# Performance work log

Measured on AMD Instinct MI355X. Metric: run time of the kernel, lower is better.

Reference implementation:

```python
import jax, jax.numpy as jnp
import numpy as np

N, D, C, G, NNZ = 256, 1024, 50000, 4, 300000
EPS = 1e-5


def setup_inputs() -> dict:
    key = jax.random.key(0)
    ks = jax.random.split(key, 5)
    return {
        "output": jax.random.normal(ks[0], (N, D), jnp.float32),
        "wt2_w": jax.random.normal(ks[1], (C, D), jnp.float32) * 0.02,
        "wt2_b": jnp.zeros((C,), jnp.float32),
        "A_vals": jax.random.uniform(ks[2], (G, NNZ), dtype=jnp.float32),
        "vec": jnp.ones((G,), jnp.float32),
        "A_rows": jax.random.randint(ks[3], (G, NNZ), 0, C, jnp.int32),
        "A_cols": jax.random.randint(ks[4], (G, NNZ), 0, C, jnp.int32),
    }


def reference(output, wt2_w, wt2_b, A_vals, vec, A_rows, A_cols):
    # BatchNorm1d(embed_dim, affine=False), training-mode batch stats (biased var)
    mean = jnp.mean(output, axis=0)
    var = jnp.var(output, axis=0)
    h0 = (output - mean) * jax.lax.rsqrt(var + EPS)
    # wt2 linear + swish -> Z [N, C]
    h1 = h0 @ wt2_w.T + wt2_b
    Z = h1 * jax.nn.sigmoid(h1)
    # multi-graph sparse propagation: neighbors += spmm(A_i * vec[i], Z^T)^T
    # spmm out[b, r] = sum_{e: rows[e]==r} vals[e] * Z[b, cols[e]]
    Zt = Z.T  # [C, N]
    neighbors = jnp.zeros_like(Z)
    n_graphs = A_vals.shape[0]
    for i in range(n_graphs):  # small fixed number of relation graphs
        vals = A_vals[i] * vec[i]               # learnable per-graph weight
        msgs = Zt[A_cols[i]] * vals[:, None]    # [nnz, N] gathered messages
        agg = jax.ops.segment_sum(msgs, A_rows[i], num_segments=Zt.shape[0])  # [C, N]
        neighbors = neighbors + agg.T
    # residual combine
    return neighbors + Z
```

## Files before the change

### kernel.cpp

```cpp
#include <hip/hip_runtime.h>

typedef __attribute__((ext_vector_type(8))) short short8;
typedef __attribute__((ext_vector_type(4))) float floatx4;

#define C_DIM 50000
#define D_DIM 1024
#define N_DIM 256
#define G_NUM 4
#define NNZ_G 300000
#define E_TOT (G_NUM * NNZ_G)

#define O_SB   0u
#define O_H0   8192u
#define O_ZT   532480u
#define O_CNT  26132480u
#define O_OFF  26332544u
#define O_CUR  26532608u
#define O_BS   26732672u
#define O_EDG  26733696u

static __device__ __forceinline__ unsigned short f2bf(float f) {
    union { float f; unsigned u; } v; v.f = f;
    unsigned r = v.u + 0x7fffu + ((v.u >> 16) & 1u);
    return (unsigned short)(r >> 16);
}
static __device__ __forceinline__ float bf2f(unsigned short u) {
    union { unsigned u; float f; } v; v.u = ((unsigned)u) << 16;
    return v.f;
}

__global__ __launch_bounds__(256) void k_bnstats(const float* __restrict__ x,
                                                 float* __restrict__ scale,
                                                 float* __restrict__ bias) {
    int d = blockIdx.x * 256 + threadIdx.x;
    float s = 0.f, ss = 0.f;
    for (int n = 0; n < N_DIM; ++n) {
        float v = x[n * D_DIM + d];
        s += v; ss += v * v;
    }
    float mean = s * (1.f / N_DIM);
    float var  = ss * (1.f / N_DIM) - mean * mean;
    float sc = rsqrtf(var + 1e-5f);
    scale[d] = sc;
    bias[d] = -mean * sc;
}

__global__ __launch_bounds__(256) void k_h0(const float* __restrict__ x,
                                            const float* __restrict__ scale,
                                            const float* __restrict__ bias,
                                            unsigned short* __restrict__ h0) {
    int id = blockIdx.x * 256 + threadIdx.x;
    int d = id & (D_DIM - 1);
    h0[id] = f2bf(x[id] * scale[d] + bias[d]);
}

__global__ __launch_bounds__(256) void k_gemm(const float* __restrict__ W,
                                              const float* __restrict__ wb,
                                              const unsigned short* __restrict__ h0,
                                              unsigned short* __restrict__ Zt) {
    __shared__ unsigned short As[64 * 40];
    __shared__ unsigned short Bs[256 * 40];
    const int t = threadIdx.x;
    const int c0 = blockIdx.x * 64;
    const int w = t >> 6, lane = t & 63;
    const int m = lane & 15, g = lane >> 4;
    const int arow = t >> 2, aseg = t & 3;

    floatx4 acc[4][4];
#pragma unroll
    for (int i = 0; i < 4; ++i)
#pragma unroll
        for (int j = 0; j < 4; ++j) acc[i][j] = (floatx4)0.f;

    for (int kk = 0; kk < D_DIM; kk += 32) {
        {
            int c = c0 + arow;
            float4 f0, f1;
            if (c < C_DIM) {
                const float4* src = (const float4*)&W[(size_t)c * D_DIM + kk + aseg * 8];
                f0 = src[0]; f1 = src[1];
            } else {
                f0 = f1 = make_float4(0.f, 0.f, 0.f, 0.f);
            }
            unsigned p0 = (unsigned)f2bf(f0.x) | ((unsigned)f2bf(f0.y) << 16);
            unsigned p1 = (unsigned)f2bf(f0.z) | ((unsigned)f2bf(f0.w) << 16);
            unsigned p2 = (unsigned)f2bf(f1.x) | ((unsigned)f2bf(f1.y) << 16);
            unsigned p3 = (unsigned)f2bf(f1.z) | ((unsigned)f2bf(f1.w) << 16);
            *(uint4*)&As[arow * 40 + aseg * 8] = make_uint4(p0, p1, p2, p3);
        }
        {
            const uint4* src = (const uint4*)&h0[(size_t)t * D_DIM + kk];
            uint4* dst = (uint4*)&Bs[t * 40];
            dst[0] = src[0]; dst[1] = src[1]; dst[2] = src[2]; dst[3] = src[3];
        }
        __syncthreads();

        short8 af[4], bfr[4];
#pragma unroll
        for (int i = 0; i < 4; ++i)
            af[i] = *(const short8*)&As[(i * 16 + m) * 40 + g * 8];
#pragma unroll
        for (int j = 0; j < 4; ++j)
            bfr[j] = *(const short8*)&Bs[(w * 64 + j * 16 + m) * 40 + g * 8];
#pragma unroll
        for (int i = 0; i < 4; ++i)
#pragma unroll
            for (int j = 0; j < 4; ++j)
                acc[i][j] = __builtin_amdgcn_mfma_f32_16x16x32_bf16(af[i], bfr[j], acc[i][j], 0, 0, 0);
        __syncthreads();
    }

#pragma unroll
    for (int i = 0; i < 4; ++i) {
#pragma unroll
        for (int j = 0; j < 4; ++j) {
            int b = w * 64 + j * 16 + m;
#pragma unroll
            for (int rr = 0; rr < 4; ++rr) {
                int c = c0 + i * 16 + g * 4 + rr;
                if (c < C_DIM) {
                    float x = acc[i][j][rr] + wb[c];
                    float z = x / (1.f + __expf(-x));
                    Zt[(size_t)c * 256 + b] = f2bf(z);
                }
            }
        }
    }
}

__global__ __launch_bounds__(256) void k_count(const int* __restrict__ rows,
                                               int* __restrict__ counts) {
    int id = blockIdx.x * 256 + threadIdx.x;
    if (id < E_TOT) atomicAdd(&counts[rows[id]], 1);
}

__global__ __launch_bounds__(256) void k_scan1(const int* __restrict__ counts,
                                               int* __restrict__ offsets,
                                               int* __restrict__ bsums) {
    __shared__ int sm[256];
    int t = threadIdx.x, i = blockIdx.x * 256 + t;
    int v = (i < C_DIM) ? counts[i] : 0;
    sm[t] = v; __syncthreads();
    for (int off = 1; off < 256; off <<= 1) {
        int x = (t >= off) ? sm[t - off] : 0;
        __syncthreads();
        sm[t] += x;
        __syncthreads();
    }
    if (i < C_DIM) offsets[i] = sm[t] - v;
    if (t == 255) bsums[blockIdx.x] = sm[255];
}

__global__ __launch_bounds__(256) void k_scan2(int* __restrict__ bsums,
                                               int* __restrict__ offsets) {
    __shared__ int sm[256];
    int t = threadIdx.x;
    int v = (t < 196) ? bsums[t] : 0;
    sm[t] = v; __syncthreads();
    for (int off = 1; off < 256; off <<= 1) {
        int x = (t >= off) ? sm[t - off] : 0;
        __syncthreads();
        sm[t] += x;
        __syncthreads();
    }
    if (t < 196) bsums[t] = sm[t] - v;
    if (t == 0) offsets[C_DIM] = sm[255];
}

__global__ __launch_bounds__(256) void k_scan3(const int* __restrict__ bsums,
                                               int* __restrict__ offsets,
                                               int* __restrict__ cursor) {
    int i = blockIdx.x * 256 + threadIdx.x;
    if (i < C_DIM) {
        int off = offsets[i] + bsums[blockIdx.x];
        offsets[i] = off;
        cursor[i] = off;
    }
}

__global__ __launch_bounds__(256) void k_scatter(const int* __restrict__ rows,
                                                 const int* __restrict__ cols,
                                                 const float* __restrict__ vals,
                                                 const float* __restrict__ vec,
                                                 int* __restrict__ cursor,
                                                 int2* __restrict__ edges) {
    int id = blockIdx.x * 256 + threadIdx.x;
    if (id < E_TOT) {
        int gidx = id / NNZ_G;
        float v = vals[id] * vec[gidx];
        int r = rows[id];
        int c = cols[id];
        int pos = atomicAdd(&cursor[r], 1);
        edges[pos] = make_int2(c, __float_as_int(v));
    }
}

__global__ __launch_bounds__(256) void k_agg(const unsigned short* __restrict__ Zt,
                                             const int* __restrict__ offsets,
                                             const int2* __restrict__ edges,
                                             float* __restrict__ out) {
    __shared__ float sm[32 * 256];
    const int t = threadIdx.x;
    const int w = t >> 6, lane = t & 63;
    const int r0 = blockIdx.x * 32;
    const int base = lane * 4;

#pragma unroll 1
    for (int k = 0; k < 8; ++k) {
        int lrow = w * 8 + k;
        int r = __builtin_amdgcn_readfirstlane(r0 + lrow);
        if (r < C_DIM) {
            ushort4 z = *(const ushort4*)&Zt[(size_t)r * 256 + base];
            float a0 = bf2f(z.x), a1 = bf2f(z.y), a2 = bf2f(z.z), a3 = bf2f(z.w);
            int s = offsets[r], e = offsets[r + 1];
            for (; s + 4 <= e; s += 4) {
                int2 e0 = edges[s], e1 = edges[s + 1], e2 = edges[s + 2], e3 = edges[s + 3];
                ushort4 g0 = *(const ushort4*)&Zt[(size_t)e0.x * 256 + base];
                ushort4 g1 = *(const ushort4*)&Zt[(size_t)e1.x * 256 + base];
                ushort4 g2 = *(const ushort4*)&Zt[(size_t)e2.x * 256 + base];
                ushort4 g3 = *(const ushort4*)&Zt[(size_t)e3.x * 256 + base];
                float v0 = __int_as_float(e0.y), v1 = __int_as_float(e1.y);
                float v2 = __int_as_float(e2.y), v3 = __int_as_float(e3.y);
                a0 += v0 * bf2f(g0.x) + v1 * bf2f(g1.x) + v2 * bf2f(g2.x) + v3 * bf2f(g3.x);
                a1 += v0 * bf2f(g0.y) + v1 * bf2f(g1.y) + v2 * bf2f(g2.y) + v3 * bf2f(g3.y);
                a2 += v0 * bf2f(g0.z) + v1 * bf2f(g1.z) + v2 * bf2f(g2.z) + v3 * bf2f(g3.z);
                a3 += v0 * bf2f(g0.w) + v1 * bf2f(g1.w) + v2 * bf2f(g2.w) + v3 * bf2f(g3.w);
            }
            for (; s < e; ++s) {
                int2 e0 = edges[s];
                ushort4 g0 = *(const ushort4*)&Zt[(size_t)e0.x * 256 + base];
                float v0 = __int_as_float(e0.y);
                a0 += v0 * bf2f(g0.x);
                a1 += v0 * bf2f(g0.y);
                a2 += v0 * bf2f(g0.z);
                a3 += v0 * bf2f(g0.w);
            }
            *(float4*)&sm[lrow * 256 + base] = make_float4(a0, a1, a2, a3);
        }
    }
    __syncthreads();

    int rows = C_DIM - r0; if (rows > 32) rows = 32;
    int nq = rows >> 2;
    float4* op = (float4*)&out[(size_t)t * C_DIM + r0];
#pragma unroll 1
    for (int q = 0; q < nq; ++q) {
        float4 o;
        o.x = sm[(q * 4 + 0) * 256 + t];
        o.y = sm[(q * 4 + 1) * 256 + t];
        o.z = sm[(q * 4 + 2) * 256 + t];
        o.w = sm[(q * 4 + 3) * 256 + t];
        op[q] = o;
    }
}

extern "C" void kernel_launch(void* const* d_in, const int* in_sizes, int n_in,
                              void* d_out, int out_size, void* d_ws, size_t ws_size,
                              hipStream_t stream) {
    (void)in_sizes; (void)n_in; (void)out_size; (void)ws_size;
    const float* x     = (const float*)d_in[0];
    const float* W     = (const float*)d_in[1];
    const float* wb    = (const float*)d_in[2];
    const float* Avals = (const float*)d_in[3];
    const float* vec   = (const float*)d_in[4];
    const int*   Arows = (const int*)d_in[5];
    const int*   Acols = (const int*)d_in[6];
    float* out = (float*)d_out;
    char* ws = (char*)d_ws;

    float* scale = (float*)(ws + O_SB);
    float* bias  = scale + 1024;
    unsigned short* h0 = (unsigned short*)(ws + O_H0);
    unsigned short* Zt = (unsigned short*)(ws + O_ZT);
    int* counts  = (int*)(ws + O_CNT);
    int* offsets = (int*)(ws + O_OFF);
    int* cursor  = (int*)(ws + O_CUR);
    int* bsums   = (int*)(ws + O_BS);
    int2* edges  = (int2*)(ws + O_EDG);

    hipMemsetAsync(counts, 0, C_DIM * sizeof(int), stream);

    k_bnstats<<<4, 256, 0, stream>>>(x, scale, bias);
    k_h0<<<1024, 256, 0, stream>>>(x, scale, bias, h0);
    k_count<<<(E_TOT + 255) / 256, 256, 0, stream>>>(Arows, counts);
    k_gemm<<<(C_DIM + 63) / 64, 256, 0, stream>>>(W, wb, h0, Zt);
    k_scan1<<<196, 256, 0, stream>>>(counts, offsets, bsums);
    k_scan2<<<1, 256, 0, stream>>>(bsums, offsets);
    k_scan3<<<196, 256, 0, stream>>>(bsums, offsets, cursor);
    k_scatter<<<(E_TOT + 255) / 256, 256, 0, stream>>>(Arows, Acols, Avals, vec, cursor, edges);
    k_agg<<<(C_DIM + 31) / 32, 256, 0, stream>>>(Zt, offsets, edges, out);
}
```

Measured before the change: 663.4 us.

## Pipeline GEMM with register prefetch and fragment-ordered h0, split agg edges across half-waves

Several changes at once. BN stats now run on more blocks with a shared-memory reduction, and h0 is written as bf16 in an MFMA-fragment order so the GEMM reads B fragments straight from global memory instead of staging them in LDS. The GEMM now double-buffers the W tile in LDS with register prefetch two steps ahead, uses raw barriers and raises wave priority around the MFMAs, which is meant to hide W load latency. In the aggregation kernel each half-wave handles alternate edges with 16-byte gathers and the halves are combined with a shuffle, giving more bytes per load and more edges in flight, at the cost of extra registers.

```diff
diff --git a/kernel.cpp b/kernel.cpp
--- a/kernel.cpp
+++ b/kernel.cpp
@@ -32,83 +32,151 @@
 __global__ __launch_bounds__(256) void k_bnstats(const float* __restrict__ x,
                                                  float* __restrict__ scale,
                                                  float* __restrict__ bias) {
-    int d = blockIdx.x * 256 + threadIdx.x;
+    __shared__ float sms[8][32], smss[8][32];
+    const int t = threadIdx.x;
+    const int dc = t & 31, grp = t >> 5;
+    const int d = blockIdx.x * 32 + dc;
     float s = 0.f, ss = 0.f;
-    for (int n = 0; n < N_DIM; ++n) {
+    for (int n = grp; n < N_DIM; n += 8) {
         float v = x[n * D_DIM + d];
         s += v; ss += v * v;
     }
-    float mean = s * (1.f / N_DIM);
-    float var  = ss * (1.f / N_DIM) - mean * mean;
-    float sc = rsqrtf(var + 1e-5f);
-    scale[d] = sc;
-    bias[d] = -mean * sc;
-}
-
-__global__ __launch_bounds__(256) void k_h0(const float* __restrict__ x,
-                                            const float* __restrict__ scale,
-                                            const float* __restrict__ bias,
-                                            unsigned short* __restrict__ h0) {
+    sms[grp][dc] = s; smss[grp][dc] = ss;
+    __syncthreads();
+    if (t < 32) {
+        float S = 0.f, SS = 0.f;
+#pragma unroll
+        for (int g2 = 0; g2 < 8; ++g2) { S += sms[g2][t]; SS += smss[g2][t]; }
+        float mean = S * (1.f / N_DIM);
+        float var  = SS * (1.f / N_DIM) - mean * mean;
+        float sc = rsqrtf(var + 1e-5f);
+        int dd = blockIdx.x * 32 + t;
+        scale[dd] = sc;
+        bias[dd] = -mean * sc;
+    }
+}
+
+__global__ __launch_bounds__(256) void k_h0f(const float* __restrict__ x,
+                                             const float* __restrict__ scale,
+                                             const float* __restrict__ bias,
+                                             unsigned short* __restrict__ h0F) {
     int id = blockIdx.x * 256 + threadIdx.x;
-    int d = id & (D_DIM - 1);
-    h0[id] = f2bf(x[id] * scale[d] + bias[d]);
+    int b = id >> 7, kc = id & 127;
+    const float4* xp = (const float4*)&x[(size_t)b * D_DIM + kc * 8];
+    float4 f0 = xp[0], f1 = xp[1];
+    const float4* sp = (const float4*)&scale[kc * 8];
+    const float4* bp = (const float4*)&bias[kc * 8];
+    float4 s0 = sp[0], s1 = sp[1], b0 = bp[0], b1 = bp[1];
+    short8 o;
+    o[0] = (short)f2bf(f0.x * s0.x + b0.x);
+    o[1] = (short)f2bf(f0.y * s0.y + b0.y);
+    o[2] = (short)f2bf(f0.z * s0.z + b0.z);
+    o[3] = (short)f2bf(f0.w * s0.w + b0.w);
+    o[4] = (short)f2bf(f1.x * s1.x + b1.x);
+    o[5] = (short)f2bf(f1.y * s1.y + b1.y);
+    o[6] = (short)f2bf(f1.z * s1.z + b1.z);
+    o[7] = (short)f2bf(f1.w * s1.w + b1.w);
+    int off = (b >> 4) * 16384 + (kc >> 2) * 512 + (kc & 3) * 128 + (b & 15) * 8;
+    *(short8*)&h0F[off] = o;
 }
 
 __global__ __launch_bounds__(256) void k_gemm(const float* __restrict__ W,
                                               const float* __restrict__ wb,
-                                              const unsigned short* __restrict__ h0,
+                                              const unsigned short* __restrict__ h0F,
                                               unsigned short* __restrict__ Zt) {
-    __shared__ unsigned short As[64 * 40];
-    __shared__ unsigned short Bs[256 * 40];
+    __shared__ unsigned short A_lds[2][8 * 64 * 8];
     const int t = threadIdx.x;
-    const int c0 = blockIdx.x * 64;
     const int w = t >> 6, lane = t & 63;
     const int m = lane & 15, g = lane >> 4;
-    const int arow = t >> 2, aseg = t & 3;
-
+    const int c0 = blockIdx.x * 64;
+
+    const int srow = t >> 4;
+    const int scc  = t & 15;
+    const int s_kh = scc >> 3;
+    const int s_g  = (scc >> 1) & 3;
+    const int s_half = scc & 1;
+    const int sbase = (srow + 16 * s_g) * 8 + s_half * 4;
+
+    const unsigned short* hb = h0F + (size_t)(w * 4) * 16384 + lane * 8;
+
+    float4 raA[4], raB[4];
     floatx4 acc[4][4];
 #pragma unroll
     for (int i = 0; i < 4; ++i)
 #pragma unroll
         for (int j = 0; j < 4; ++j) acc[i][j] = (floatx4)0.f;
 
-    for (int kk = 0; kk < D_DIM; kk += 32) {
-        {
-            int c = c0 + arow;
-            float4 f0, f1;
-            if (c < C_DIM) {
-                const float4* src = (const float4*)&W[(size_t)c * D_DIM + kk + aseg * 8];
-                f0 = src[0]; f1 = src[1];
-            } else {
-                f0 = f1 = make_float4(0.f, 0.f, 0.f, 0.f);
-            }
-            unsigned p0 = (unsigned)f2bf(f0.x) | ((unsigned)f2bf(f0.y) << 16);
-            unsigned p1 = (unsigned)f2bf(f0.z) | ((unsigned)f2bf(f0.w) << 16);
-            unsigned p2 = (unsigned)f2bf(f1.x) | ((unsigned)f2bf(f1.y) << 16);
-            unsigned p3 = (unsigned)f2bf(f1.z) | ((unsigned)f2bf(f1.w) << 16);
-            *(uint4*)&As[arow * 40 + aseg * 8] = make_uint4(p0, p1, p2, p3);
-        }
-        {
-            const uint4* src = (const uint4*)&h0[(size_t)t * D_DIM + kk];
-            uint4* dst = (uint4*)&Bs[t * 40];
-            dst[0] = src[0]; dst[1] = src[1]; dst[2] = src[2]; dst[3] = src[3];
-        }
-        __syncthreads();
-
-        short8 af[4], bfr[4];
-#pragma unroll
-        for (int i = 0; i < 4; ++i)
-            af[i] = *(const short8*)&As[(i * 16 + m) * 40 + g * 8];
-#pragma unroll
-        for (int j = 0; j < 4; ++j)
-            bfr[j] = *(const short8*)&Bs[(w * 64 + j * 16 + m) * 40 + g * 8];
-#pragma unroll
-        for (int i = 0; i < 4; ++i)
-#pragma unroll
-            for (int j = 0; j < 4; ++j)
-                acc[i][j] = __builtin_amdgcn_mfma_f32_16x16x32_bf16(af[i], bfr[j], acc[i][j], 0, 0, 0);
-        __syncthreads();
-    }
+#define LOADA(RA, ksv)                                                           \
+    {                                                                            \
+        const int kkv = (ksv) * 64;                                              \
+        _Pragma("unroll")                                                        \
+        for (int q = 0; q < 4; ++q) {                                            \
+            int rr_ = c0 + q * 16 + srow; if (rr_ >= C_DIM) rr_ = C_DIM - 1;     \
+            RA[q] = *(const float4*)&W[(size_t)rr_ * D_DIM + kkv + scc * 4];     \
+        }                                                                        \
+    }
+#define STOREA(RA, bufv)                                                          \
+    {                                                                             \
+        _Pragma("unroll")                                                         \
+        for (int q = 0; q < 4; ++q) {                                             \
+            float4 f_ = RA[q];                                                    \
+            unsigned p0_ = (unsigned)f2bf(f_.x) | ((unsigned)f2bf(f_.y) << 16);   \
+            unsigned p1_ = (unsigned)f2bf(f_.z) | ((unsigned)f2bf(f_.w) << 16);   \
+            *(uint2*)&A_lds[bufv][(s_kh * 4 + q) * 512 + sbase] =                 \
+                make_uint2(p0_, p1_);                                             \
+        }                                                                         \
+    }
+#define BARRIER()                                               \
+    asm volatile("s_waitcnt lgkmcnt(0)" ::: "memory");          \
+    __builtin_amdgcn_sched_barrier(0);                          \
+    __builtin_amdgcn_s_barrier();                               \
+    __builtin_amdgcn_sched_barrier(0);
+
+#define GSTEP(ksv, RAs, RAl, CUR)                                                 \
+    {                                                                             \
+        short8 bfrag[2][4];                                                       \
+        _Pragma("unroll")                                                         \
+        for (int kh = 0; kh < 2; ++kh)                                            \
+            _Pragma("unroll")                                                     \
+            for (int j = 0; j < 4; ++j)                                           \
+                bfrag[kh][j] = *(const short8*)&hb[(size_t)j * 16384 +            \
+                                                  ((ksv) * 2 + kh) * 512];        \
+        short8 afrag[2][4];                                                       \
+        _Pragma("unroll")                                                         \
+        for (int kh = 0; kh < 2; ++kh)                                            \
+            _Pragma("unroll")                                                     \
+            for (int i = 0; i < 4; ++i)                                           \
+                afrag[kh][i] = *(const short8*)&A_lds[CUR][(kh * 4 + i) * 512 +   \
+                                                          lane * 8];              \
+        if ((ksv) < 15) STOREA(RAs, (CUR) ^ 1)                                    \
+        if ((ksv) < 14) LOADA(RAl, (ksv) + 2)                                     \
+        __builtin_amdgcn_s_setprio(1);                                            \
+        _Pragma("unroll")                                                         \
+        for (int kh = 0; kh < 2; ++kh)                                            \
+            _Pragma("unroll")                                                     \
+            for (int i = 0; i < 4; ++i)                                           \
+                _Pragma("unroll")                                                 \
+                for (int j = 0; j < 4; ++j)                                       \
+                    acc[i][j] = __builtin_amdgcn_mfma_f32_16x16x32_bf16(          \
+                        afrag[kh][i], bfrag[kh][j], acc[i][j], 0, 0, 0);          \
+        __builtin_amdgcn_s_setprio(0);                                            \
+        BARRIER()                                                                 \
+    }
+
+    LOADA(raA, 0)
+    STOREA(raA, 0)
+    LOADA(raB, 1)
+    BARRIER()
+
+#pragma unroll 1
+    for (int ks2 = 0; ks2 < 16; ks2 += 2) {
+        GSTEP(ks2,     raB, raA, 0)
+        GSTEP(ks2 + 1, raA, raB, 1)
+    }
+#undef GSTEP
+#undef LOADA
+#undef STOREA
+#undef BARRIER
 
 #pragma unroll
     for (int i = 0; i < 4; ++i) {
@@ -203,39 +271,55 @@
     const int t = threadIdx.x;
     const int w = t >> 6, lane = t & 63;
     const int r0 = blockIdx.x * 32;
-    const int base = lane * 4;
+    const int h = lane & 31;
+    const int eh = lane >> 5;
+    const int base = h * 8;
 
 #pragma unroll 1
     for (int k = 0; k < 8; ++k) {
         int lrow = w * 8 + k;
         int r = __builtin_amdgcn_readfirstlane(r0 + lrow);
         if (r < C_DIM) {
-            ushort4 z = *(const ushort4*)&Zt[(size_t)r * 256 + base];
-            float a0 = bf2f(z.x), a1 = bf2f(z.y), a2 = bf2f(z.z), a3 = bf2f(z.w);
+            float a[8];
+            {
+                short8 z = *(const short8*)&Zt[(size_t)r * 256 + base];
+                float zm = eh ? 0.f : 1.f;
+#pragma unroll
+                for (int j = 0; j < 8; ++j) a[j] = zm * bf2f((unsigned short)z[j]);
+            }
             int s = offsets[r], e = offsets[r + 1];
             for (; s + 4 <= e; s += 4) {
-                int2 e0 = edges[s], e1 = edges[s + 1], e2 = edges[s + 2], e3 = edges[s + 3];
-                ushort4 g0 = *(const ushort4*)&Zt[(size_t)e0.x * 256 + base];
-                ushort4 g1 = *(const ushort4*)&Zt[(size_t)e1.x * 256 + base];
-                ushort4 g2 = *(const ushort4*)&Zt[(size_t)e2.x * 256 + base];
-                ushort4 g3 = *(const ushort4*)&Zt[(size_t)e3.x * 256 + base];
-                float v0 = __int_as_float(e0.y), v1 = __int_as_float(e1.y);
-                float v2 = __int_as_float(e2.y), v3 = __int_as_float(e3.y);
-                a0 += v0 * bf2f(g0.x) + v1 * bf2f(g1.x) + v2 * bf2f(g2.x) + v3 * bf2f(g3.x);
-                a1 += v0 * bf2f(g0.y) + v1 * bf2f(g1.y) + v2 * bf2f(g2.y) + v3 * bf2f(g3.y);
-                a2 += v0 * bf2f(g0.z) + v1 * bf2f(g1.z) + v2 * bf2f(g2.z) + v3 * bf2f(g3.z);
-                a3 += v0 * bf2f(g0.w) + v1 * bf2f(g1.w) + v2 * bf2f(g2.w) + v3 * bf2f(g3.w);
-            }
-            for (; s < e; ++s) {
+                int2 ea = edges[s + eh];
+                int2 eb = edges[s + 2 + eh];
+                short8 ga = *(const short8*)&Zt[(size_t)(unsigned)ea.x * 256 + base];
+                short8 gb = *(const short8*)&Zt[(size_t)(unsigned)eb.x * 256 + base];
+                float va = __int_as_float(ea.y), vb = __int_as_float(eb.y);
+#pragma unroll
+                for (int j = 0; j < 8; ++j)
+                    a[j] += va * bf2f((unsigned short)ga[j]) + vb * bf2f((unsigned short)gb[j]);
+            }
+            for (; s + 2 <= e; s += 2) {
+                int2 ea = edges[s + eh];
+                short8 ga = *(const short8*)&Zt[(size_t)(unsigned)ea.x * 256 + base];
+                float va = __int_as_float(ea.y);
+#pragma unroll
+                for (int j = 0; j < 8; ++j)
+                    a[j] += va * bf2f((unsigned short)ga[j]);
+            }
+            if (s < e) {
                 int2 e0 = edges[s];
-                ushort4 g0 = *(const ushort4*)&Zt[(size_t)e0.x * 256 + base];
-                float v0 = __int_as_float(e0.y);
-                a0 += v0 * bf2f(g0.x);
-                a1 += v0 * bf2f(g0.y);
-                a2 += v0 * bf2f(g0.z);
-                a3 += v0 * bf2f(g0.w);
-            }
-            *(float4*)&sm[lrow * 256 + base] = make_float4(a0, a1, a2, a3);
+                short8 g0 = *(const short8*)&Zt[(size_t)(unsigned)e0.x * 256 + base];
+                float v0 = eh ? 0.f : __int_as_float(e0.y);
+#pragma unroll
+                for (int j = 0; j < 8; ++j)
+                    a[j] += v0 * bf2f((unsigned short)g0[j]);
+            }
+#pragma unroll
+            for (int j = 0; j < 8; ++j) a[j] += __shfl_xor(a[j], 32);
+            if (eh == 0) {
+                *(float4*)&sm[lrow * 256 + base]     = make_float4(a[0], a[1], a[2], a[3]);
+                *(float4*)&sm[lrow * 256 + base + 4] = make_float4(a[4], a[5], a[6], a[7]);
+            }
         }
     }
     __syncthreads();
@@ -270,8 +354,8 @@
 
     float* scale = (float*)(ws + O_SB);
     float* bias  = scale + 1024;
-    unsigned short* h0 = (unsigned short*)(ws + O_H0);
-    unsigned short* Zt = (unsigned short*)(ws + O_ZT);
+    unsigned short* h0F = (unsigned short*)(ws + O_H0);
+    unsigned short* Zt  = (unsigned short*)(ws + O_ZT);
     int* counts  = (int*)(ws + O_CNT);
     int* offsets = (int*)(ws + O_OFF);
     int* cursor  = (int*)(ws + O_CUR);
@@ -280,10 +364,10 @@
 
     hipMemsetAsync(counts, 0, C_DIM * sizeof(int), stream);
 
-    k_bnstats<<<4, 256, 0, stream>>>(x, scale, bias);
-    k_h0<<<1024, 256, 0, stream>>>(x, scale, bias, h0);
+    k_bnstats<<<32, 256, 0, stream>>>(x, scale, bias);
+    k_h0f<<<128, 256, 0, stream>>>(x, scale, bias, h0F);
     k_count<<<(E_TOT + 255) / 256, 256, 0, stream>>>(Arows, counts);
-    k_gemm<<<(C_DIM + 63) / 64, 256, 0, stream>>>(W, wb, h0, Zt);
+    k_gemm<<<(C_DIM + 63) / 64, 256, 0, stream>>>(W, wb, h0F, Zt);
     k_scan1<<<196, 256, 0, stream>>>(counts, offsets, bsums);
     k_scan2<<<1, 256, 0, stream>>>(bsums, offsets);
     k_scan3<<<196, 256, 0, stream>>>(bsums, offsets, cursor);
```

After: 625.1 us. 5.8% less time.
